# Kernel optimization log

Measured on AMD Instinct MI355X. Metric: run time of the kernel, lower is better.

Reference implementation:

```python
import jax, jax.numpy as jnp
import numpy as np

C = 512
NUM_HEADS = 8
GROUPS = min(32, C // 4)
EPS = 1e-5
SCALE = (C // NUM_HEADS) ** (-0.5)


def setup_inputs() -> dict:
    key = jax.random.key(0)
    ks = jax.random.split(key, 7)
    B, H, W = 8, 32, 32
    x = jax.random.normal(ks[0], (B, C, H, W), dtype=jnp.float32)
    gamma = jnp.ones((C,), dtype=jnp.float32)
    beta = jnp.zeros((C,), dtype=jnp.float32)
    # 1x1 convs == per-pixel matmuls; store weights as [out, in]
    w_qkv = jax.random.normal(ks[1], (3 * C, C), dtype=jnp.float32) * (C ** -0.5)
    b_qkv = jax.random.normal(ks[2], (3 * C,), dtype=jnp.float32) * 0.01
    w_proj = jax.random.normal(ks[3], (C, C), dtype=jnp.float32) * (C ** -0.5)
    b_proj = jax.random.normal(ks[4], (C,), dtype=jnp.float32) * 0.01
    return {"x": x, "gamma": gamma, "beta": beta, "w_qkv": w_qkv,
            "b_qkv": b_qkv, "w_proj": w_proj, "b_proj": b_proj}


def _group_norm(x, gamma, beta):
    B, Cc, H, W = x.shape
    xg = x.reshape(B, GROUPS, Cc // GROUPS, H, W)
    mean = jnp.mean(xg, axis=(2, 3, 4), keepdims=True)
    var = jnp.var(xg, axis=(2, 3, 4), keepdims=True)
    xg = (xg - mean) * jax.lax.rsqrt(var + EPS)
    x = xg.reshape(B, Cc, H, W)
    return x * gamma[None, :, None, None] + beta[None, :, None, None]


def reference(x, gamma, beta, w_qkv, b_qkv, w_proj, b_proj):
    B, Cc, H, W = x.shape
    nh, hd = NUM_HEADS, Cc // NUM_HEADS
    HW = H * W
    h = _group_norm(x, gamma, beta)
    # 1x1 conv: [B,C,H,W] -> [B,3C,H,W]
    qkv = jnp.einsum('oc,bchw->bohw', w_qkv, h) + b_qkv[None, :, None, None]
    qkv = qkv.reshape(B, 3, nh, hd, HW)
    q, k, v = qkv[:, 0], qkv[:, 1], qkv[:, 2]  # each [B, nh, hd, HW]
    scores = jnp.einsum('bhcq,bhck->bhqk', q, k) * SCALE  # [B, nh, HW, HW]
    attn = jax.nn.softmax(scores, axis=-1)
    out = jnp.einsum('bhqk,bhck->bhcq', attn, v)  # [B, nh, hd, HW]
    out = out.reshape(B, Cc, H, W)
    out = jnp.einsum('oc,bchw->bohw', w_proj, out) + b_proj[None, :, None, None]
    return x + out
```

## Files before the change

### kernel.cpp

```cpp
#include <hip/hip_runtime.h>
#include <stdint.h>
#include <math.h>

#define CDIM 512
#define NHEAD 8
#define HD 64
#define HWD 1024
#define BATCH 8
#define NGRP 32
#define CPG 16
#define EPSV 1e-5f
#define QSCALE 0.125f

typedef __bf16 bf16x8 __attribute__((ext_vector_type(8)));
typedef float f32x4 __attribute__((ext_vector_type(4)));

static __device__ __forceinline__ unsigned short f2bf(float x){
  union { float f; unsigned u; } v; v.f = x;
  unsigned r = v.u + 0x7fffu + ((v.u >> 16) & 1u);
  return (unsigned short)(r >> 16);
}

static __device__ __forceinline__ void gload_lds16(const void* g, void* l){
  __builtin_amdgcn_global_load_lds(
      (const __attribute__((address_space(1))) unsigned int*)g,
      (__attribute__((address_space(3))) unsigned int*)l, 16, 0, 0);
}

__global__ void cvt2_kernel(const float* __restrict__ a, const float* __restrict__ b,
                            unsigned short* __restrict__ oa, unsigned short* __restrict__ ob,
                            int na, int nb){
  int i = (blockIdx.x * blockDim.x + threadIdx.x) * 4;
  const float* src; unsigned short* dst; int j;
  if (i < na){ src = a; dst = oa; j = i; }
  else { j = i - na; if (j >= nb) return; src = b; dst = ob; }
  float4 v = *(const float4*)(src + j);
  ushort4 o;
  o.x = f2bf(v.x); o.y = f2bf(v.y); o.z = f2bf(v.z); o.w = f2bf(v.w);
  *(ushort4*)(dst + j) = o;
}

__global__ __launch_bounds__(256) void gn_kernel(const float* __restrict__ x,
    const float* __restrict__ gamma, const float* __restrict__ beta,
    unsigned short* __restrict__ hT){
  int b   = blockIdx.x >> 5;
  int grp = blockIdx.x & 31;
  int c0  = grp * CPG;
  int t   = threadIdx.x;
  const float* xp = x + ((size_t)b * CDIM + c0) * HWD;
  float vals[CPG][4];
  float s = 0.f, s2 = 0.f;
  #pragma unroll
  for (int j = 0; j < CPG; ++j){
    #pragma unroll
    for (int k = 0; k < 4; ++k){
      float v = xp[j * HWD + t + 256 * k];
      vals[j][k] = v; s += v; s2 += v * v;
    }
  }
  #pragma unroll
  for (int off = 32; off > 0; off >>= 1){
    s  += __shfl_down(s, off);
    s2 += __shfl_down(s2, off);
  }
  __shared__ float red[8];
  __shared__ float stats[2];
  int lane = t & 63, wid = t >> 6;
  if (lane == 0){ red[wid] = s; red[wid + 4] = s2; }
  __syncthreads();
  if (t == 0){
    float ts  = red[0] + red[1] + red[2] + red[3];
    float ts2 = red[4] + red[5] + red[6] + red[7];
    float mean = ts * (1.f / (CPG * HWD));
    float var  = ts2 * (1.f / (CPG * HWD)) - mean * mean;
    stats[0] = mean; stats[1] = rsqrtf(var + EPSV);
  }
  __syncthreads();
  float mean = stats[0], inv = stats[1];
  float gm[CPG], bt[CPG];
  #pragma unroll
  for (int j = 0; j < CPG; ++j){ gm[j] = gamma[c0 + j] * inv; bt[j] = beta[c0 + j]; }
  #pragma unroll
  for (int k = 0; k < 4; ++k){
    unsigned pk[8];
    #pragma unroll
    for (int j = 0; j < 8; ++j){
      unsigned short lo = f2bf((vals[2*j][k]   - mean) * gm[2*j]   + bt[2*j]);
      unsigned short hi = f2bf((vals[2*j+1][k] - mean) * gm[2*j+1] + bt[2*j+1]);
      pk[j] = (unsigned)lo | ((unsigned)hi << 16);
    }
    size_t base = ((size_t)b * HWD + t + 256 * k) * CDIM + c0;
    uint4 a0 = {pk[0], pk[1], pk[2], pk[3]};
    uint4 a1 = {pk[4], pk[5], pk[6], pk[7]};
    *(uint4*)(hT + base)     = a0;
    *(uint4*)(hT + base + 8) = a1;
  }
}

template<int MODE>
__global__ __launch_bounds__(256) void gemm_bt(
    const unsigned short* __restrict__ A,
    const unsigned short* __restrict__ BT,
    const float* __restrict__ bias,
    const float* __restrict__ xres,
    float* __restrict__ outf,
    unsigned short* __restrict__ qT,
    unsigned short* __restrict__ kT,
    unsigned short* __restrict__ vb,
    int M, int N, int K)
{
  __shared__ unsigned short As[128*64];
  __shared__ unsigned short Bs[128*64];
  int n0 = blockIdx.x * 128;
  int m0 = blockIdx.y * 128;
  int b  = blockIdx.z;
  int t  = threadIdx.x;
  int lane = t & 63, wid = t >> 6;
  int wr = wid >> 1, wc = wid & 1;
  int lr = lane & 15, g = lane >> 4;
  const unsigned short* Bb = BT + (size_t)b * N * K;

  int srow = wid * 32 + (lane >> 3);
  int sseg = (lane & 7) ^ (lane >> 3);
  const unsigned short* ag = A  + (size_t)(m0 + srow) * K + sseg * 8;
  const unsigned short* bg = Bb + (size_t)(n0 + srow) * K + sseg * 8;

  f32x4 acc[4][4];
  f32x4 zz = {0.f, 0.f, 0.f, 0.f};
  #pragma unroll
  for (int m = 0; m < 4; ++m)
    #pragma unroll
    for (int n = 0; n < 4; ++n) acc[m][n] = zz;

  for (int k0 = 0; k0 < K; k0 += 64){
    #pragma unroll
    for (int j = 0; j < 4; ++j){
      gload_lds16(ag + (size_t)j*8*K + k0, &As[(wid*32 + j*8)*64]);
      gload_lds16(bg + (size_t)j*8*K + k0, &Bs[(wid*32 + j*8)*64]);
    }
    __syncthreads();
    #pragma unroll
    for (int kk = 0; kk < 2; ++kk){
      unsigned segx = (unsigned)(((kk*4 + g) ^ (lr & 7)) << 4);
      bf16x8 af[4], bfr[4];
      #pragma unroll
      for (int m = 0; m < 4; ++m)
        af[m] = *(const bf16x8*)((const char*)As + (unsigned)((wr*64 + m*16 + lr)*128) + segx);
      #pragma unroll
      for (int n = 0; n < 4; ++n)
        bfr[n] = *(const bf16x8*)((const char*)Bs + (unsigned)((wc*64 + n*16 + lr)*128) + segx);
      #pragma unroll
      for (int m = 0; m < 4; ++m)
        #pragma unroll
        for (int n = 0; n < 4; ++n)
          acc[m][n] = __builtin_amdgcn_mfma_f32_16x16x32_bf16(af[m], bfr[n], acc[m][n], 0, 0, 0);
    }
    __syncthreads();
  }

  if (MODE == 0){
    #pragma unroll
    for (int m = 0; m < 4; ++m){
      int o_base = m0 + wr*64 + m*16 + g*4;
      int s = o_base >> 9;
      int h = (o_base >> 6) & 7;
      int dbase = o_base & 63;
      float bv[4];
      #pragma unroll
      for (int r = 0; r < 4; ++r) bv[r] = bias[o_base + r];
      #pragma unroll
      for (int n = 0; n < 4; ++n){
        int hw = n0 + wc*64 + n*16 + lr;
        if (s == 2){
          int a = hw & 31;
          int hwp = (hw & ~31) | (((a >> 2) & 3) * 8 + (a & 3) + (((a >> 4) & 1) << 2));
          #pragma unroll
          for (int r = 0; r < 4; ++r){
            float val = acc[m][n][r] + bv[r];
            vb[(((size_t)b*NHEAD + h)*HD + dbase + r)*HWD + hwp] = f2bf(val);
          }
        } else {
          float sc = (s == 0) ? QSCALE : 1.f;
          ushort4 pk;
          pk.x = f2bf((acc[m][n][0] + bv[0]) * sc);
          pk.y = f2bf((acc[m][n][1] + bv[1]) * sc);
          pk.z = f2bf((acc[m][n][2] + bv[2]) * sc);
          pk.w = f2bf((acc[m][n][3] + bv[3]) * sc);
          unsigned short* dst = (s == 0) ? qT : kT;
          *(ushort4*)&dst[(((size_t)b*NHEAD + h)*HWD + hw)*HD + dbase] = pk;
        }
      }
    }
  } else {
    #pragma unroll
    for (int m = 0; m < 4; ++m){
      int o0 = m0 + wr*64 + m*16 + g*4;
      #pragma unroll
      for (int n = 0; n < 4; ++n){
        int hw = n0 + wc*64 + n*16 + lr;
        #pragma unroll
        for (int r = 0; r < 4; ++r){
          int o = o0 + r;
          size_t idx = ((size_t)b * M + o) * N + hw;
          outf[idx] = acc[m][n][r] + bias[o] + xres[idx];
        }
      }
    }
  }
}

__global__ __launch_bounds__(512, 2) void attn_flash(
    const unsigned short* __restrict__ qT,
    const unsigned short* __restrict__ kT,
    const unsigned short* __restrict__ vperm,
    unsigned short* __restrict__ aoT)
{
  __shared__ char smem[65536];
  int bh = blockIdx.x;
  int b = bh >> 3, h = bh & 7;
  int t = threadIdx.x;
  int lane = t & 63, wid = t >> 6;
  int lr = lane & 15, g = lane >> 4;
  int q0 = blockIdx.y * 256 + wid * 32;

  const unsigned short* qp = qT + ((size_t)bh * HWD + q0) * HD;
  const unsigned short* kp = kT + (size_t)bh * HWD * HD;
  const unsigned short* vp = vperm + (size_t)bh * HD * HWD;

  int krl  = lane >> 3;
  int kseg = (lane & 7) ^ krl;
  const unsigned short* kg = kp + (size_t)(wid*16 + krl) * HD + kseg * 8;
  unsigned kdst = (unsigned)(wid * 16 * 128);
  int vrl = lane >> 4;

  bf16x8 yq[2][2];
  #pragma unroll
  for (int qt = 0; qt < 2; ++qt){
    yq[qt][0] = *(const bf16x8*)&qp[(qt*16 + lr)*HD + g*8];
    yq[qt][1] = *(const bf16x8*)&qp[(qt*16 + lr)*HD + 32 + g*8];
  }

  f32x4 accO[2][4];
  f32x4 zz = {0.f, 0.f, 0.f, 0.f};
  #pragma unroll
  for (int qt = 0; qt < 2; ++qt)
    #pragma unroll
    for (int dt = 0; dt < 4; ++dt) accO[qt][dt] = zz;
  float mrun[2] = {-1e30f, -1e30f};
  float lrun[2] = {0.f, 0.f};

  #pragma unroll
  for (int j = 0; j < 2; ++j){
    gload_lds16(kg + (size_t)j*8*HD, smem + kdst + j*8*128);
    int vrow = wid*8 + j*4 + vrl;
    int vseg = (lane & 15) ^ (vrow & 15);
    gload_lds16(vp + (size_t)vrow*HWD + vseg*8,
                smem + 16384u + (unsigned)vrow*256u);
  }
  __syncthreads();

  unsigned cur = 0;
  for (int kc = 0; kc < 8; ++kc){
    if (kc < 7){
      char* bufn = smem + (cur^1u)*32768u;
      int c1 = kc + 1;
      #pragma unroll
      for (int j = 0; j < 2; ++j){
        gload_lds16(kg + ((size_t)c1*128 + j*8)*HD, bufn + kdst + j*8*128);
        int vrow = wid*8 + j*4 + vrl;
        int vseg = (lane & 15) ^ (vrow & 15);
        gload_lds16(vp + (size_t)vrow*HWD + c1*128 + vseg*8,
                    bufn + 16384u + (unsigned)vrow*256u);
      }
    }

    char* kbuf = smem + cur*32768u;
    char* vbuf = kbuf + 16384;

    f32x4 s[2][8];
    __builtin_amdgcn_s_setprio(1);
    #pragma unroll
    for (int tt = 0; tt < 8; ++tt){
      unsigned rb = (unsigned)((tt*16 + lr) * 128);
      bf16x8 k0 = *(const bf16x8*)(kbuf + rb + (((g    ) ^ (lr&7)) << 4));
      bf16x8 k1 = *(const bf16x8*)(kbuf + rb + (((4 + g) ^ (lr&7)) << 4));
      #pragma unroll
      for (int qt = 0; qt < 2; ++qt){
        f32x4 z = zz;
        z = __builtin_amdgcn_mfma_f32_16x16x32_bf16(k0, yq[qt][0], z, 0, 0, 0);
        s[qt][tt] = __builtin_amdgcn_mfma_f32_16x16x32_bf16(k1, yq[qt][1], z, 0, 0, 0);
      }
    }
    __builtin_amdgcn_s_setprio(0);

    #pragma unroll
    for (int qt = 0; qt < 2; ++qt){
      float cm = -1e30f;
      #pragma unroll
      for (int tt = 0; tt < 8; ++tt)
        #pragma unroll
        for (int r = 0; r < 4; ++r) cm = fmaxf(cm, s[qt][tt][r]);
      cm = fmaxf(cm, __shfl_xor(cm, 16));
      cm = fmaxf(cm, __shfl_xor(cm, 32));

      float mn = fmaxf(mrun[qt], cm);
      float f  = __expf(mrun[qt] - mn);
      mrun[qt] = mn;

      float ps = 0.f;
      #pragma unroll
      for (int tt = 0; tt < 8; ++tt)
        #pragma unroll
        for (int r = 0; r < 4; ++r){
          float e = __expf(s[qt][tt][r] - mn);
          s[qt][tt][r] = e; ps += e;
        }
      ps += __shfl_xor(ps, 16);
      ps += __shfl_xor(ps, 32);
      lrun[qt] = lrun[qt] * f + ps;

      float fD[4];
      #pragma unroll
      for (int r = 0; r < 4; ++r) fD[r] = __shfl(f, g*4 + r);
      #pragma unroll
      for (int dt = 0; dt < 4; ++dt)
        #pragma unroll
        for (int r = 0; r < 4; ++r) accO[qt][dt][r] *= fD[r];
    }

    __builtin_amdgcn_s_setprio(1);
    #pragma unroll
    for (int mi = 0; mi < 4; ++mi){
      bf16x8 xp[2];
      #pragma unroll
      for (int qt = 0; qt < 2; ++qt)
        #pragma unroll
        for (int j = 0; j < 4; ++j){
          xp[qt][j]     = (__bf16)s[qt][2*mi][j];
          xp[qt][4 + j] = (__bf16)s[qt][2*mi + 1][j];
        }
      #pragma unroll
      for (int dt = 0; dt < 4; ++dt){
        unsigned rb = (unsigned)((dt*16 + lr) * 256) + (unsigned)((((mi*4 + g) ^ lr) & 15) << 4);
        bf16x8 yv = *(const bf16x8*)(vbuf + rb);
        #pragma unroll
        for (int qt = 0; qt < 2; ++qt)
          accO[qt][dt] = __builtin_amdgcn_mfma_f32_16x16x32_bf16(xp[qt], yv, accO[qt][dt], 0, 0, 0);
      }
    }
    __builtin_amdgcn_s_setprio(0);

    __syncthreads();
    cur ^= 1u;
  }

  #pragma unroll
  for (int qt = 0; qt < 2; ++qt){
    float invl = 1.f / lrun[qt];
    float ir[4];
    #pragma unroll
    for (int r = 0; r < 4; ++r) ir[r] = __shfl(invl, g*4 + r);
    #pragma unroll
    for (int dt = 0; dt < 4; ++dt)
      #pragma unroll
      for (int r = 0; r < 4; ++r){
        int qi = q0 + qt*16 + g*4 + r;
        aoT[((size_t)b*HWD + qi)*CDIM + h*HD + dt*16 + lr] = f2bf(accO[qt][dt][r] * ir[r]);
      }
  }
}

extern "C" void kernel_launch(void* const* d_in, const int* in_sizes, int n_in,
                              void* d_out, int out_size, void* d_ws, size_t ws_size,
                              hipStream_t stream) {
  const float* x      = (const float*)d_in[0];
  const float* gamma  = (const float*)d_in[1];
  const float* beta   = (const float*)d_in[2];
  const float* w_qkv  = (const float*)d_in[3];
  const float* b_qkv  = (const float*)d_in[4];
  const float* w_proj = (const float*)d_in[5];
  const float* b_proj = (const float*)d_in[6];
  float* out = (float*)d_out;

  char* ws = (char*)d_ws;
  size_t off = 0;
  unsigned short* wqkv_b  = (unsigned short*)(ws + off); off += (size_t)1536*512*2;
  unsigned short* wproj_b = (unsigned short*)(ws + off); off += (size_t)512*512*2;
  unsigned short* hT      = (unsigned short*)(ws + off); off += (size_t)BATCH*HWD*CDIM*2;
  unsigned short* qT      = (unsigned short*)(ws + off); off += (size_t)BATCH*NHEAD*HWD*HD*2;
  unsigned short* kT      = (unsigned short*)(ws + off); off += (size_t)BATCH*NHEAD*HWD*HD*2;
  unsigned short* vb      = (unsigned short*)(ws + off); off += (size_t)BATCH*NHEAD*HWD*HD*2;
  unsigned short* aoT     = hT;

  cvt2_kernel<<<1024, 256, 0, stream>>>(w_qkv, w_proj, wqkv_b, wproj_b, 1536*512, 512*512);

  gn_kernel<<<BATCH*NGRP, 256, 0, stream>>>(x, gamma, beta, hT);

  gemm_bt<0><<<dim3(HWD/128, 1536/128, BATCH), 256, 0, stream>>>(
      wqkv_b, hT, b_qkv, nullptr, nullptr, qT, kT, vb, 1536, HWD, CDIM);

  attn_flash<<<dim3(BATCH*NHEAD, HWD/256), 512, 0, stream>>>(qT, kT, vb, aoT);

  gemm_bt<1><<<dim3(HWD/128, CDIM/128, BATCH), 256, 0, stream>>>(
      wproj_b, aoT, b_proj, x, out, nullptr, nullptr, nullptr, CDIM, HWD, CDIM);
}
```

Measured before the change: 84.61 us.

## Fuse weight conversion into groupnorm launch and transpose PV MFMA output layout

Merges the weight bf16 conversion and the groupnorm into one launch. Extra blocks handle the conversion, which saves a kernel launch and lets both jobs overlap. The groupnorm now reads float4-vectorized contiguous pixels instead of strided scalars. In attention, the PV MFMA operands are swapped so each lane holds a row of the output. This removes the cross-lane shuffles for rescale factors and the final normalization, and allows packed 8-byte stores of the output instead of scalar 2-byte stores.

Measured after the change: 80.53 us, median of 3. 1.05x faster.

```diff
diff --git a/kernel.cpp b/kernel.cpp
--- a/kernel.cpp
+++ b/kernel.cpp
@@ -27,36 +27,43 @@
       (__attribute__((address_space(3))) unsigned int*)l, 16, 0, 0);
 }
 
-__global__ void cvt2_kernel(const float* __restrict__ a, const float* __restrict__ b,
-                            unsigned short* __restrict__ oa, unsigned short* __restrict__ ob,
-                            int na, int nb){
-  int i = (blockIdx.x * blockDim.x + threadIdx.x) * 4;
-  const float* src; unsigned short* dst; int j;
-  if (i < na){ src = a; dst = oa; j = i; }
-  else { j = i - na; if (j >= nb) return; src = b; dst = ob; }
-  float4 v = *(const float4*)(src + j);
-  ushort4 o;
-  o.x = f2bf(v.x); o.y = f2bf(v.y); o.z = f2bf(v.z); o.w = f2bf(v.w);
-  *(ushort4*)(dst + j) = o;
-}
-
-__global__ __launch_bounds__(256) void gn_kernel(const float* __restrict__ x,
+__global__ __launch_bounds__(256) void gncvt_kernel(
+    const float* __restrict__ x,
     const float* __restrict__ gamma, const float* __restrict__ beta,
-    unsigned short* __restrict__ hT){
-  int b   = blockIdx.x >> 5;
-  int grp = blockIdx.x & 31;
+    unsigned short* __restrict__ hT,
+    const float* __restrict__ wa, const float* __restrict__ wb,
+    unsigned short* __restrict__ oa, unsigned short* __restrict__ ob,
+    int na, int nb)
+{
+  int bid = blockIdx.x;
+  int t   = threadIdx.x;
+  if (bid >= BATCH * NGRP){
+    int cb = bid - BATCH * NGRP;
+    #pragma unroll
+    for (int it = 0; it < 4; ++it){
+      int i = (cb * 1024 + it * 256 + t) * 4;
+      const float* src; unsigned short* dst; int j;
+      if (i < na){ src = wa; dst = oa; j = i; }
+      else { j = i - na; if (j >= nb) return; src = wb; dst = ob; }
+      float4 v = *(const float4*)(src + j);
+      ushort4 o;
+      o.x = f2bf(v.x); o.y = f2bf(v.y); o.z = f2bf(v.z); o.w = f2bf(v.w);
+      *(ushort4*)(dst + j) = o;
+    }
+    return;
+  }
+  int b   = bid >> 5;
+  int grp = bid & 31;
   int c0  = grp * CPG;
-  int t   = threadIdx.x;
   const float* xp = x + ((size_t)b * CDIM + c0) * HWD;
-  float vals[CPG][4];
+  f32x4 vals[CPG];
   float s = 0.f, s2 = 0.f;
   #pragma unroll
   for (int j = 0; j < CPG; ++j){
-    #pragma unroll
-    for (int k = 0; k < 4; ++k){
-      float v = xp[j * HWD + t + 256 * k];
-      vals[j][k] = v; s += v; s2 += v * v;
-    }
+    f32x4 v = *(const f32x4*)(xp + j * HWD + t * 4);
+    vals[j] = v;
+    #pragma unroll
+    for (int k = 0; k < 4; ++k){ s += v[k]; s2 += v[k] * v[k]; }
   }
   #pragma unroll
   for (int off = 32; off > 0; off >>= 1){
@@ -89,7 +96,7 @@
       unsigned short hi = f2bf((vals[2*j+1][k] - mean) * gm[2*j+1] + bt[2*j+1]);
       pk[j] = (unsigned)lo | ((unsigned)hi << 16);
     }
-    size_t base = ((size_t)b * HWD + t + 256 * k) * CDIM + c0;
+    size_t base = ((size_t)b * HWD + t * 4 + k) * CDIM + c0;
     uint4 a0 = {pk[0], pk[1], pk[2], pk[3]};
     uint4 a1 = {pk[4], pk[5], pk[6], pk[7]};
     *(uint4*)(hT + base)     = a0;
@@ -319,13 +326,10 @@
       ps += __shfl_xor(ps, 32);
       lrun[qt] = lrun[qt] * f + ps;
 
-      float fD[4];
-      #pragma unroll
-      for (int r = 0; r < 4; ++r) fD[r] = __shfl(f, g*4 + r);
       #pragma unroll
       for (int dt = 0; dt < 4; ++dt)
         #pragma unroll
-        for (int r = 0; r < 4; ++r) accO[qt][dt][r] *= fD[r];
+        for (int r = 0; r < 4; ++r) accO[qt][dt][r] *= f;
     }
 
     __builtin_amdgcn_s_setprio(1);
@@ -345,7 +349,7 @@
         bf16x8 yv = *(const bf16x8*)(vbuf + rb);
         #pragma unroll
         for (int qt = 0; qt < 2; ++qt)
-          accO[qt][dt] = __builtin_amdgcn_mfma_f32_16x16x32_bf16(xp[qt], yv, accO[qt][dt], 0, 0, 0);
+          accO[qt][dt] = __builtin_amdgcn_mfma_f32_16x16x32_bf16(yv, xp[qt], accO[qt][dt], 0, 0, 0);
       }
     }
     __builtin_amdgcn_s_setprio(0);
@@ -357,16 +361,16 @@
   #pragma unroll
   for (int qt = 0; qt < 2; ++qt){
     float invl = 1.f / lrun[qt];
-    float ir[4];
-    #pragma unroll
-    for (int r = 0; r < 4; ++r) ir[r] = __shfl(invl, g*4 + r);
-    #pragma unroll
-    for (int dt = 0; dt < 4; ++dt)
-      #pragma unroll
-      for (int r = 0; r < 4; ++r){
-        int qi = q0 + qt*16 + g*4 + r;
-        aoT[((size_t)b*HWD + qi)*CDIM + h*HD + dt*16 + lr] = f2bf(accO[qt][dt][r] * ir[r]);
-      }
+    size_t rowb = ((size_t)b * HWD + q0 + qt*16 + lr) * CDIM + h*HD;
+    #pragma unroll
+    for (int dt = 0; dt < 4; ++dt){
+      ushort4 pk;
+      pk.x = f2bf(accO[qt][dt][0] * invl);
+      pk.y = f2bf(accO[qt][dt][1] * invl);
+      pk.z = f2bf(accO[qt][dt][2] * invl);
+      pk.w = f2bf(accO[qt][dt][3] * invl);
+      *(ushort4*)&aoT[rowb + dt*16 + g*4] = pk;
+    }
   }
 }
 
@@ -392,9 +396,8 @@
   unsigned short* vb      = (unsigned short*)(ws + off); off += (size_t)BATCH*NHEAD*HWD*HD*2;
   unsigned short* aoT     = hT;
 
-  cvt2_kernel<<<1024, 256, 0, stream>>>(w_qkv, w_proj, wqkv_b, wproj_b, 1536*512, 512*512);
-
-  gn_kernel<<<BATCH*NGRP, 256, 0, stream>>>(x, gamma, beta, hT);
+  gncvt_kernel<<<512, 256, 0, stream>>>(x, gamma, beta, hT,
+      w_qkv, w_proj, wqkv_b, wproj_b, 1536*512, 512*512);
 
   gemm_bt<0><<<dim3(HWD/128, 1536/128, BATCH), 256, 0, stream>>>(
       wqkv_b, hT, b_qkv, nullptr, nullptr, qT, kT, vb, 1536, HWD, CDIM);
```
